# Performance work log

Measured on AMD Instinct MI355X. Metric: run time of the kernel, lower is better.

Reference implementation:

```python
import jax, jax.numpy as jnp
import numpy as np

EPS = 1e-8  # torch F.cosine_similarity eps


def setup_inputs() -> dict:
    key = jax.random.key(0)
    x = jax.random.normal(key, (16, 256, 2048), dtype=jnp.float32)
    return {"x": x}


def reference(x) -> jnp.ndarray:
    # x: [b, c, p]. Pairwise cosine similarity between point columns, diag = 1.
    # Equivalent to the original O(p) loop of F.cosine_similarity calls,
    # fused into one batched matmul.
    b, c, p = x.shape
    dots = jnp.einsum("bcp,bcq->bpq", x, x)            # [b, p, p]
    norms = jnp.sqrt(jnp.sum(x * x, axis=1))            # [b, p]
    denom = jnp.maximum(norms[:, :, None] * norms[:, None, :], EPS)
    sim = dots / denom
    eye = jnp.eye(p, dtype=x.dtype)
    res = jnp.where(eye[None, :, :] > 0, jnp.ones((), x.dtype), sim)
    return res
```

## Files before the change

kernel.cpp:

```cpp
#include <hip/hip_runtime.h>

#define B_ 16
#define C_ 256
#define P_ 2048
#define BK 32
#define KT 8

typedef __attribute__((ext_vector_type(8))) short short8;
typedef __attribute__((ext_vector_type(4))) float floatx4;

__device__ inline short f2bf(float v) {
  union { float f; unsigned u; } c; c.f = v;
  unsigned r = c.u + 0x7fffu + ((c.u >> 16) & 1u);
  return (short)(r >> 16);
}

#define GLOAD_LDS16(g, l)                                          \
  __builtin_amdgcn_global_load_lds(                                \
      (const __attribute__((address_space(1))) void*)(g),          \
      (__attribute__((address_space(3))) void*)(l), 16, 0, 0)

__global__ __launch_bounds__(256, 4) void k_transpose(const float* __restrict__ x,
                                                      short* __restrict__ Xt,
                                                      float* __restrict__ nrm2p) {
  __shared__ float t[2][32][133];
  __shared__ float red[8][32][4];
  const int p0 = blockIdx.x * 128, b = blockIdx.y, zc = blockIdx.z;
  const float* xb = x + (size_t)b * C_ * P_;
  short* xtb = Xt + (size_t)b * P_ * C_;
  const int tid = threadIdx.x;
  const int tx = tid & 31;
  const int cg = tid >> 5;
  floatx4 s4 = (floatx4){0.f, 0.f, 0.f, 0.f};
  const int cbase = zc * 128;
#pragma unroll 1
  for (int chunk = 0; chunk < 4; ++chunk) {
    const int c0 = cbase + chunk * 32;
    const int tb = chunk & 1;
    float4 v[4];
#pragma unroll
    for (int i = 0; i < 4; ++i)
      v[i] = *reinterpret_cast<const float4*>(&xb[(size_t)(c0 + cg + i * 8) * P_ + p0 + tx * 4]);
#pragma unroll
    for (int i = 0; i < 4; ++i) {
      *reinterpret_cast<float4*>(&t[tb][cg + i * 8][tx * 4]) = v[i];
      s4[0] += v[i].x * v[i].x;
      s4[1] += v[i].y * v[i].y;
      s4[2] += v[i].z * v[i].z;
      s4[3] += v[i].w * v[i].w;
    }
    __syncthreads();
#pragma unroll
    for (int u = 0; u < 4; ++u) {
      const int unit = tid + 256 * u;
      const int r = unit >> 3, ch = unit & 7;
      short4 w;
      w.x = f2bf(t[tb][ch * 4 + 0][r]);
      w.y = f2bf(t[tb][ch * 4 + 1][r]);
      w.z = f2bf(t[tb][ch * 4 + 2][r]);
      w.w = f2bf(t[tb][ch * 4 + 3][r]);
      *reinterpret_cast<short4*>(&xtb[(size_t)(p0 + r) * C_ + c0 + ch * 4]) = w;
    }
  }
  *reinterpret_cast<floatx4*>(&red[cg][tx][0]) = s4;
  __syncthreads();
  if (tid < 128) {
    const int cgp = tid >> 2, j = tid & 3;
    float ns = 0.f;
#pragma unroll
    for (int g = 0; g < 8; ++g) ns += red[g][cgp][j];
    nrm2p[(size_t)zc * B_ * P_ + b * P_ + p0 + tid] = ns;
  }
}

__global__ __launch_bounds__(256, 4) void k_gemm(const short* __restrict__ Xt,
                                                 const float* __restrict__ nrm2p,
                                                 float* __restrict__ out) {
  const int bid = blockIdx.x;
  const int xcd = bid & 7;
  const int s = bid >> 3;
  const int b = xcd * 2 + (s >> 8);
  const int t = s & 255;
  const int tm = t >> 4, tn = t & 15;
  const int p0 = tm * 128, q0 = tn * 128;
  const short* Xb = Xt + (size_t)b * P_ * C_;

  __shared__ __align__(16) char smem[32768];

  const int tid = threadIdx.x;
  const int lane = tid & 63;
  const int wid = tid >> 6;
  const int wrow = wid >> 1;
  const int wcol = wid & 1;

  floatx4 acc[4][4];
#pragma unroll
  for (int i = 0; i < 4; ++i)
#pragma unroll
    for (int j = 0; j < 4; ++j) acc[i][j] = (floatx4){0.f, 0.f, 0.f, 0.f};

  const int K2 = C_ * 2;

  auto STAGE = [&](int buf, int kt) {
    const int kb = kt * (BK * 2);
#pragma unroll
    for (int j = 0; j < 2; ++j) {
      const int chunk = j * 4 + wid;
      const int f = chunk * 1024 + lane * 16;
      const int row = f >> 6;
      const int inrow = f & 63;
      GLOAD_LDS16((const char*)Xb + (size_t)(p0 + row) * K2 + kb + inrow,
                  smem + buf * 8192 + chunk * 1024);
      GLOAD_LDS16((const char*)Xb + (size_t)(q0 + row) * K2 + kb + inrow,
                  smem + 16384 + buf * 8192 + chunk * 1024);
    }
  };

  STAGE(0, 0);

  for (int kt = 0; kt < KT; ++kt) {
    const int cur = kt & 1;
    if (kt < KT - 1) {
      STAGE(cur ^ 1, kt + 1);
      asm volatile("s_waitcnt vmcnt(4)\n\ts_barrier" ::: "memory");
    } else {
      asm volatile("s_waitcnt vmcnt(0)\n\ts_barrier" ::: "memory");
    }

    const short* As = (const short*)(smem + cur * 8192);
    const short* Bs = (const short*)(smem + 16384 + cur * 8192);
    short8 af[4], bf[4];
#pragma unroll
    for (int mi = 0; mi < 4; ++mi) {
      const int r = wrow * 64 + mi * 16 + (lane & 15);
      af[mi] = *reinterpret_cast<const short8*>(&As[r * BK + (lane >> 4) * 8]);
    }
#pragma unroll
    for (int ni = 0; ni < 4; ++ni) {
      const int r = wcol * 64 + ni * 16 + (lane & 15);
      bf[ni] = *reinterpret_cast<const short8*>(&Bs[r * BK + (lane >> 4) * 8]);
    }
#pragma unroll
    for (int mi = 0; mi < 4; ++mi)
#pragma unroll
      for (int ni = 0; ni < 4; ++ni)
        acc[mi][ni] = __builtin_amdgcn_mfma_f32_16x16x32_bf16(af[mi], bf[ni], acc[mi][ni], 0, 0, 0);

    asm volatile("s_waitcnt lgkmcnt(0)\n\ts_barrier" ::: "memory");
  }

  const float* n2a = nrm2p + (size_t)b * P_;
  const float* n2b = nrm2p + (size_t)B_ * P_ + (size_t)b * P_;
  float* ob = out + (size_t)b * P_ * P_;
  const int cl = lane & 15, rg4 = (lane >> 4) * 4;

  float rnq[4];
#pragma unroll
  for (int ni = 0; ni < 4; ++ni) {
    const int qc = q0 + wcol * 64 + ni * 16 + cl;
    rnq[ni] = __builtin_amdgcn_rcpf(fmaxf(sqrtf(n2a[qc] + n2b[qc]), 1e-4f));
  }
  floatx4 rnp[4];
#pragma unroll
  for (int mi = 0; mi < 4; ++mi) {
    const int pb = p0 + wrow * 64 + mi * 16 + rg4;
    const float4 pa = *reinterpret_cast<const float4*>(&n2a[pb]);
    const float4 pbv = *reinterpret_cast<const float4*>(&n2b[pb]);
    rnp[mi][0] = __builtin_amdgcn_rcpf(fmaxf(sqrtf(pa.x + pbv.x), 1e-4f));
    rnp[mi][1] = __builtin_amdgcn_rcpf(fmaxf(sqrtf(pa.y + pbv.y), 1e-4f));
    rnp[mi][2] = __builtin_amdgcn_rcpf(fmaxf(sqrtf(pa.z + pbv.z), 1e-4f));
    rnp[mi][3] = __builtin_amdgcn_rcpf(fmaxf(sqrtf(pa.w + pbv.w), 1e-4f));
  }

#pragma unroll
  for (int mi = 0; mi < 4; ++mi) {
    const int prow = p0 + wrow * 64 + mi * 16 + rg4;
#pragma unroll
    for (int ni = 0; ni < 4; ++ni) {
      floatx4 vv = acc[mi][ni] * rnp[mi] * rnq[ni];
      const int qc = q0 + wcol * 64 + ni * 16 + cl;
      if (tm == tn) {
        const int d = qc - prow;
        if (d >= 0 && d < 4) vv[d] = 1.0f;
      }
      ob[(size_t)(prow + 0) * P_ + qc] = vv[0];
      ob[(size_t)(prow + 1) * P_ + qc] = vv[1];
      ob[(size_t)(prow + 2) * P_ + qc] = vv[2];
      ob[(size_t)(prow + 3) * P_ + qc] = vv[3];
    }
  }
}

extern "C" void kernel_launch(void* const* d_in, const int* in_sizes, int n_in,
                              void* d_out, int out_size, void* d_ws, size_t ws_size,
                              hipStream_t stream) {
  const float* x = (const float*)d_in[0];
  float* out = (float*)d_out;

  short* Xt = (short*)d_ws;
  float* nrm2p = (float*)((char*)d_ws + (size_t)B_ * P_ * C_ * sizeof(short));

  k_transpose<<<dim3(P_ / 128, B_, 2), 256, 0, stream>>>(x, Xt, nrm2p);
  k_gemm<<<dim3(16 * 16 * B_), 256, 0, stream>>>(Xt, nrm2p, out);
}
```

Measured before the change: 84.65 us.

## Fuse transpose, bf16 conversion and norm computation into the GEMM kernel

Removes the separate transpose kernel and its bf16 workspace. The GEMM now reads fp32 x directly through register prefetch, converts it to bf16 into double-buffered LDS, and accumulates per-column squared norms on the fly. Norms are reduced across waves in LDS before the epilogue. This saves one launch and the workspace round trip, but each tile re-reads fp32 inputs (16x redundancy across tiles), which doubles the bytes per load compared with bf16. It also replaces the async global-to-LDS loads with register staging and lowers occupancy to 3 blocks.

```diff
diff --git a/kernel.cpp b/kernel.cpp
--- a/kernel.cpp
+++ b/kernel.cpp
@@ -3,7 +3,6 @@
 #define B_ 16
 #define C_ 256
 #define P_ 2048
-#define BK 32
 #define KT 8
 
 typedef __attribute__((ext_vector_type(8))) short short8;
@@ -15,67 +14,8 @@
   return (short)(r >> 16);
 }
 
-#define GLOAD_LDS16(g, l)                                          \
-  __builtin_amdgcn_global_load_lds(                                \
-      (const __attribute__((address_space(1))) void*)(g),          \
-      (__attribute__((address_space(3))) void*)(l), 16, 0, 0)
-
-__global__ __launch_bounds__(256, 4) void k_transpose(const float* __restrict__ x,
-                                                      short* __restrict__ Xt,
-                                                      float* __restrict__ nrm2p) {
-  __shared__ float t[2][32][133];
-  __shared__ float red[8][32][4];
-  const int p0 = blockIdx.x * 128, b = blockIdx.y, zc = blockIdx.z;
-  const float* xb = x + (size_t)b * C_ * P_;
-  short* xtb = Xt + (size_t)b * P_ * C_;
-  const int tid = threadIdx.x;
-  const int tx = tid & 31;
-  const int cg = tid >> 5;
-  floatx4 s4 = (floatx4){0.f, 0.f, 0.f, 0.f};
-  const int cbase = zc * 128;
-#pragma unroll 1
-  for (int chunk = 0; chunk < 4; ++chunk) {
-    const int c0 = cbase + chunk * 32;
-    const int tb = chunk & 1;
-    float4 v[4];
-#pragma unroll
-    for (int i = 0; i < 4; ++i)
-      v[i] = *reinterpret_cast<const float4*>(&xb[(size_t)(c0 + cg + i * 8) * P_ + p0 + tx * 4]);
-#pragma unroll
-    for (int i = 0; i < 4; ++i) {
-      *reinterpret_cast<float4*>(&t[tb][cg + i * 8][tx * 4]) = v[i];
-      s4[0] += v[i].x * v[i].x;
-      s4[1] += v[i].y * v[i].y;
-      s4[2] += v[i].z * v[i].z;
-      s4[3] += v[i].w * v[i].w;
-    }
-    __syncthreads();
-#pragma unroll
-    for (int u = 0; u < 4; ++u) {
-      const int unit = tid + 256 * u;
-      const int r = unit >> 3, ch = unit & 7;
-      short4 w;
-      w.x = f2bf(t[tb][ch * 4 + 0][r]);
-      w.y = f2bf(t[tb][ch * 4 + 1][r]);
-      w.z = f2bf(t[tb][ch * 4 + 2][r]);
-      w.w = f2bf(t[tb][ch * 4 + 3][r]);
-      *reinterpret_cast<short4*>(&xtb[(size_t)(p0 + r) * C_ + c0 + ch * 4]) = w;
-    }
-  }
-  *reinterpret_cast<floatx4*>(&red[cg][tx][0]) = s4;
-  __syncthreads();
-  if (tid < 128) {
-    const int cgp = tid >> 2, j = tid & 3;
-    float ns = 0.f;
-#pragma unroll
-    for (int g = 0; g < 8; ++g) ns += red[g][cgp][j];
-    nrm2p[(size_t)zc * B_ * P_ + b * P_ + p0 + tid] = ns;
-  }
-}
-
-__global__ __launch_bounds__(256, 4) void k_gemm(const short* __restrict__ Xt,
-                                                 const float* __restrict__ nrm2p,
-                                                 float* __restrict__ out) {
+__global__ __launch_bounds__(256, 3) void k_fused(const float* __restrict__ x,
+                                                  float* __restrict__ out) {
   const int bid = blockIdx.x;
   const int xcd = bid & 7;
   const int s = bid >> 3;
@@ -83,9 +23,11 @@
   const int t = s & 255;
   const int tm = t >> 4, tn = t & 15;
   const int p0 = tm * 128, q0 = tn * 128;
-  const short* Xb = Xt + (size_t)b * P_ * C_;
+  const float* xb = x + (size_t)b * C_ * P_;
 
-  __shared__ __align__(16) char smem[32768];
+  __shared__ __align__(16) short As[2][128 * 32];
+  __shared__ __align__(16) short Bs[2][128 * 32];
+  __shared__ float pn[4][256];
 
   const int tid = threadIdx.x;
   const int lane = tid & 63;
@@ -99,77 +41,89 @@
 #pragma unroll
     for (int j = 0; j < 4; ++j) acc[i][j] = (floatx4){0.f, 0.f, 0.f, 0.f};
 
-  const int K2 = C_ * 2;
+  float av[2][8], bv[2][8];
+  float nsA[2] = {0.f, 0.f}, nsB[2] = {0.f, 0.f};
 
-  auto STAGE = [&](int buf, int kt) {
-    const int kb = kt * (BK * 2);
-#pragma unroll
-    for (int j = 0; j < 2; ++j) {
-      const int chunk = j * 4 + wid;
-      const int f = chunk * 1024 + lane * 16;
-      const int row = f >> 6;
-      const int inrow = f & 63;
-      GLOAD_LDS16((const char*)Xb + (size_t)(p0 + row) * K2 + kb + inrow,
-                  smem + buf * 8192 + chunk * 1024);
-      GLOAD_LDS16((const char*)Xb + (size_t)(q0 + row) * K2 + kb + inrow,
-                  smem + 16384 + buf * 8192 + chunk * 1024);
-    }
-  };
+#define LOADS(kt_)                                                        \
+  do {                                                                    \
+    const int cb_ = (kt_)*32 + wid * 8;                                   \
+    _Pragma("unroll") for (int j = 0; j < 8; ++j) {                       \
+      av[0][j] = xb[(size_t)(cb_ + j) * P_ + p0 + lane];                  \
+      av[1][j] = xb[(size_t)(cb_ + j) * P_ + p0 + 64 + lane];             \
+      bv[0][j] = xb[(size_t)(cb_ + j) * P_ + q0 + lane];                  \
+      bv[1][j] = xb[(size_t)(cb_ + j) * P_ + q0 + 64 + lane];             \
+    }                                                                     \
+  } while (0)
 
-  STAGE(0, 0);
+  LOADS(0);
 
   for (int kt = 0; kt < KT; ++kt) {
     const int cur = kt & 1;
-    if (kt < KT - 1) {
-      STAGE(cur ^ 1, kt + 1);
-      asm volatile("s_waitcnt vmcnt(4)\n\ts_barrier" ::: "memory");
-    } else {
-      asm volatile("s_waitcnt vmcnt(0)\n\ts_barrier" ::: "memory");
+#pragma unroll
+    for (int tt = 0; tt < 2; ++tt) {
+      short8 sa, sb;
+      float na = 0.f, nb = 0.f;
+#pragma unroll
+      for (int j = 0; j < 8; ++j) {
+        const float a_ = av[tt][j], b_ = bv[tt][j];
+        sa[j] = f2bf(a_);
+        sb[j] = f2bf(b_);
+        na += a_ * a_;
+        nb += b_ * b_;
+      }
+      nsA[tt] += na;
+      nsB[tt] += nb;
+      const int row = tt * 64 + lane;
+      *reinterpret_cast<short8*>(&As[cur][row * 32 + wid * 8]) = sa;
+      *reinterpret_cast<short8*>(&Bs[cur][row * 32 + wid * 8]) = sb;
     }
+    if (kt < KT - 1) LOADS(kt + 1);
 
-    const short* As = (const short*)(smem + cur * 8192);
-    const short* Bs = (const short*)(smem + 16384 + cur * 8192);
+    asm volatile("s_waitcnt lgkmcnt(0)\n\ts_barrier" ::: "memory");
+
     short8 af[4], bf[4];
 #pragma unroll
     for (int mi = 0; mi < 4; ++mi) {
       const int r = wrow * 64 + mi * 16 + (lane & 15);
-      af[mi] = *reinterpret_cast<const short8*>(&As[r * BK + (lane >> 4) * 8]);
+      af[mi] = *reinterpret_cast<const short8*>(&As[cur][r * 32 + (lane >> 4) * 8]);
     }
 #pragma unroll
     for (int ni = 0; ni < 4; ++ni) {
       const int r = wcol * 64 + ni * 16 + (lane & 15);
-      bf[ni] = *reinterpret_cast<const short8*>(&Bs[r * BK + (lane >> 4) * 8]);
+      bf[ni] = *reinterpret_cast<const short8*>(&Bs[cur][r * 32 + (lane >> 4) * 8]);
     }
 #pragma unroll
     for (int mi = 0; mi < 4; ++mi)
 #pragma unroll
       for (int ni = 0; ni < 4; ++ni)
         acc[mi][ni] = __builtin_amdgcn_mfma_f32_16x16x32_bf16(af[mi], bf[ni], acc[mi][ni], 0, 0, 0);
-
-    asm volatile("s_waitcnt lgkmcnt(0)\n\ts_barrier" ::: "memory");
   }
 
-  const float* n2a = nrm2p + (size_t)b * P_;
-  const float* n2b = nrm2p + (size_t)B_ * P_ + (size_t)b * P_;
+  pn[wid][lane] = nsA[0];
+  pn[wid][64 + lane] = nsA[1];
+  pn[wid][128 + lane] = nsB[0];
+  pn[wid][192 + lane] = nsB[1];
+  asm volatile("s_waitcnt lgkmcnt(0)\n\ts_barrier" ::: "memory");
+
   float* ob = out + (size_t)b * P_ * P_;
   const int cl = lane & 15, rg4 = (lane >> 4) * 4;
 
   float rnq[4];
 #pragma unroll
   for (int ni = 0; ni < 4; ++ni) {
-    const int qc = q0 + wcol * 64 + ni * 16 + cl;
-    rnq[ni] = __builtin_amdgcn_rcpf(fmaxf(sqrtf(n2a[qc] + n2b[qc]), 1e-4f));
+    const int qr = wcol * 64 + ni * 16 + cl;
+    const float n2 = pn[0][128 + qr] + pn[1][128 + qr] + pn[2][128 + qr] + pn[3][128 + qr];
+    rnq[ni] = __builtin_amdgcn_rcpf(fmaxf(sqrtf(n2), 1e-4f));
   }
   floatx4 rnp[4];
 #pragma unroll
   for (int mi = 0; mi < 4; ++mi) {
-    const int pb = p0 + wrow * 64 + mi * 16 + rg4;
-    const float4 pa = *reinterpret_cast<const float4*>(&n2a[pb]);
-    const float4 pbv = *reinterpret_cast<const float4*>(&n2b[pb]);
-    rnp[mi][0] = __builtin_amdgcn_rcpf(fmaxf(sqrtf(pa.x + pbv.x), 1e-4f));
-    rnp[mi][1] = __builtin_amdgcn_rcpf(fmaxf(sqrtf(pa.y + pbv.y), 1e-4f));
-    rnp[mi][2] = __builtin_amdgcn_rcpf(fmaxf(sqrtf(pa.z + pbv.z), 1e-4f));
-    rnp[mi][3] = __builtin_amdgcn_rcpf(fmaxf(sqrtf(pa.w + pbv.w), 1e-4f));
+#pragma unroll
+    for (int r = 0; r < 4; ++r) {
+      const int pr = wrow * 64 + mi * 16 + rg4 + r;
+      const float n2 = pn[0][pr] + pn[1][pr] + pn[2][pr] + pn[3][pr];
+      rnp[mi][r] = __builtin_amdgcn_rcpf(fmaxf(sqrtf(n2), 1e-4f));
+    }
   }
 
 #pragma unroll
@@ -196,10 +150,5 @@
                               hipStream_t stream) {
   const float* x = (const float*)d_in[0];
   float* out = (float*)d_out;
-
-  short* Xt = (short*)d_ws;
-  float* nrm2p = (float*)((char*)d_ws + (size_t)B_ * P_ * C_ * sizeof(short));
-
-  k_transpose<<<dim3(P_ / 128, B_, 2), 256, 0, stream>>>(x, Xt, nrm2p);
-  k_gemm<<<dim3(16 * 16 * B_), 256, 0, stream>>>(Xt, nrm2p, out);
+  k_fused<<<dim3(16 * 16 * B_), 256, 0, stream>>>(x, out);
 }
```

After: 107.4 us. 26.9% more time.
